# Optimization experiments

Measured on AMD Instinct MI355X. Metric: run time of the kernel, lower is better.

## Reference

```python
import jax, jax.numpy as jnp
import numpy as np

B, N, D, H, K = 32, 256, 256, 8, 16
EPS = 1e-8
SINK_EPS = 1e-6
SINK_ITERS = 10
TAU_SLOT = 0.5
G_TEMP = 1.0
FROB_LAMBDA = 0.02
ORTH_LAMBDA = 0.1
USAGE_LAMBDA = 0.1


def _xavier(key, shape, fan_in, fan_out):
    bound = np.sqrt(6.0 / (fan_in + fan_out))
    return jax.random.uniform(key, shape, jnp.float32, -bound, bound)


def setup_inputs() -> dict:
    key = jax.random.key(0)
    k0, k1, k2, k3, k4 = jax.random.split(key, 5)
    return {
        "desc_embeddings": jax.random.normal(k0, (B, N, D), jnp.float32),
        "name_value_embeddings": jax.random.normal(k1, (B, N, D), jnp.float32),
        "W_fusion": _xavier(k2, (D, 2 * D), 2 * D, D),   # torch Linear weight [out,in]
        "b_fusion": jnp.zeros((D,), jnp.float32),
        "W_slot": _xavier(k3, (K, D), D, K),
        "b_slot": jnp.zeros((K,), jnp.float32),
        "G_param": _xavier(k4, (H, K, K), K * K, H * K),
    }


def _sinkhorn(M, iters=SINK_ITERS, eps=SINK_EPS):
    M = jnp.maximum(M, eps)
    for _ in range(iters):  # fixed small iter count
        M = M / (M.sum(axis=-1, keepdims=True) + eps)
        M = M / (M.sum(axis=-2, keepdims=True) + eps)
    return M


def _forward(desc, nv, W_fusion, b_fusion, W_slot, b_slot, G_param):
    # fusion + slot assignment  S: [B,N,K]
    z = jnp.concatenate([desc, nv], axis=-1) @ W_fusion.T + b_fusion
    S = jax.nn.softmax(z @ W_slot.T + b_slot, axis=-1)

    # global slot-transition matrices  G: [H,K,K]
    G = jax.nn.softmax(G_param / G_TEMP, axis=-1)
    G = _sinkhorn(G)
    G = G * (1.0 - jnp.eye(K, dtype=G.dtype))  # zero diagonal

    # Frobenius diversity regularizer across heads
    V = G.reshape(H, -1)
    V = V / jnp.maximum(jnp.linalg.norm(V, axis=1, keepdims=True), 1e-8)
    Gram = V @ V.T
    g_reg = FROB_LAMBDA * (Gram.sum() - jnp.trace(Gram)) / (H * (H - 1))

    # slot-bilinear affinity  A: [B,H,N,N]
    SG = jnp.einsum('bnk,hkl->bhnl', S, G)
    A_slot = jnp.einsum('bhnl,bml->bhnm', SG, S)
    Q = jax.nn.softmax(A_slot / max(TAU_SLOT, 1e-6), axis=-1)

    # slot orthogonality regularizer
    StS = jnp.einsum('bnk,bnl->bkl', S, S) / float(N)
    offdiag = StS * (1.0 - jnp.eye(K, dtype=S.dtype))
    reg_orth = ORTH_LAMBDA * jnp.mean(offdiag ** 2)

    # slot usage KL(u || uniform)
    u = S.mean(axis=1)
    u = u / (u.sum(axis=-1, keepdims=True) + EPS)
    uc = jnp.maximum(u, EPS)
    usage_kl = jnp.mean(jnp.sum(uc * (jnp.log(uc) - jnp.log(jnp.float32(1.0 / K))), axis=-1))
    reg_usage = USAGE_LAMBDA * usage_kl

    total_reg = reg_orth + reg_usage + g_reg
    bias_log = jax.lax.stop_gradient(jnp.log(jnp.maximum(Q, EPS)))
    return bias_log, Q, total_reg


def reference(desc_embeddings, name_value_embeddings, W_fusion, b_fusion, W_slot, b_slot, G_param):
    return _forward(desc_embeddings, name_value_embeddings, W_fusion, b_fusion, W_slot, b_slot, G_param)
```

## Files before the change

kernel.cpp:

```cpp
#include <hip/hip_runtime.h>
#include <math.h>

#define LOG_EPS   (-18.420680743952367f)
#define LOG_INV_K (-2.772588722239781f)

__global__ void kA(const float* __restrict__ W_fusion, const float* __restrict__ b_fusion,
                   const float* __restrict__ W_slot,   const float* __restrict__ b_slot,
                   const float* __restrict__ G_param,
                   float* __restrict__ W_eff, float* __restrict__ b_eff,
                   float* __restrict__ G_out, float* __restrict__ out_reg) {
    int t = threadIdx.x;
    if (blockIdx.x < 32) {
        int idx = blockIdx.x * 256 + t;
        int k = idx >> 9, j = idx & 511;
        const float* ws = W_slot + k * 256;
        float s = 0.f;
        #pragma unroll 4
        for (int d = 0; d < 256; ++d) s += ws[d] * W_fusion[d * 512 + j];
        W_eff[idx] = s;
        if (idx < 16) {
            float bb = b_slot[idx];
            for (int d = 0; d < 256; ++d) bb += W_slot[idx * 256 + d] * b_fusion[d];
            b_eff[idx] = bb;
        }
        return;
    }
    __shared__ float M[2048];
    __shared__ float red[256];
    __shared__ float inv_nrm[8];
    __shared__ float hsq[8];
    __shared__ float trace_s;

    if (t < 128) {
        int base = t * 16;
        float v[16]; float mx = -1e30f;
        #pragma unroll
        for (int l = 0; l < 16; ++l) { v[l] = G_param[base + l]; mx = fmaxf(mx, v[l]); }
        float s = 0.f;
        #pragma unroll
        for (int l = 0; l < 16; ++l) { v[l] = expf(v[l] - mx); s += v[l]; }
        float r = 1.f / s;
        #pragma unroll
        for (int l = 0; l < 16; ++l) M[base + l] = fmaxf(v[l] * r, 1e-6f);
    }
    __syncthreads();
    for (int it = 0; it < 10; ++it) {
        if (t < 128) {
            float s = 0.f;
            #pragma unroll
            for (int l = 0; l < 16; ++l) s += M[t * 16 + l];
            float r = 1.f / (s + 1e-6f);
            #pragma unroll
            for (int l = 0; l < 16; ++l) M[t * 16 + l] *= r;
        }
        __syncthreads();
        if (t < 128) {
            int h = t >> 4, l = t & 15, base = h * 256 + l;
            float s = 0.f;
            #pragma unroll
            for (int k = 0; k < 16; ++k) s += M[base + k * 16];
            float r = 1.f / (s + 1e-6f);
            #pragma unroll
            for (int k = 0; k < 16; ++k) M[base + k * 16] *= r;
        }
        __syncthreads();
    }
    if (t < 128) { int h = t >> 4, k = t & 15; M[h * 256 + k * 16 + k] = 0.f; }
    __syncthreads();
    for (int i = t; i < 2048; i += 256) G_out[i] = M[i];

    if (t < 128) {
        float s = 0.f;
        #pragma unroll
        for (int l = 0; l < 16; ++l) { float x = M[t * 16 + l]; s += x * x; }
        red[t] = s;
    }
    __syncthreads();
    if (t < 8) {
        float s = 0.f;
        for (int k = 0; k < 16; ++k) s += red[t * 16 + k];
        float inv = 1.f / fmaxf(sqrtf(s), 1e-8f);
        inv_nrm[t] = inv;
        hsq[t] = s * inv * inv;
    }
    __syncthreads();
    if (t == 0) {
        float tr = 0.f;
        for (int h = 0; h < 8; ++h) tr += hsq[h];
        trace_s = tr;
    }
    __syncthreads();
    float w = 0.f;
    #pragma unroll
    for (int h = 0; h < 8; ++h) w += M[h * 256 + t] * inv_nrm[h];
    red[t] = w * w;
    __syncthreads();
    for (int off = 128; off; off >>= 1) {
        if (t < off) red[t] += red[t + off];
        __syncthreads();
    }
    if (t == 0) out_reg[0] = 0.02f * (red[0] - trace_s) / 56.f;
}

__global__ void kB(const float* __restrict__ desc, const float* __restrict__ nv,
                   const float* __restrict__ W_eff, const float* __restrict__ b_eff,
                   float* __restrict__ S) {
    int row  = blockIdx.x * 4 + (threadIdx.x >> 6);
    int lane = threadIdx.x & 63;
    int k = lane & 15, q = lane >> 4;
    const float* x = (q < 2) ? (desc + (size_t)row * 256 + q * 128)
                             : (nv   + (size_t)row * 256 + (q - 2) * 128);
    const float4* x4 = (const float4*)x;
    const float4* w4 = (const float4*)(W_eff + k * 512 + q * 128);
    float acc = 0.f;
    #pragma unroll
    for (int i = 0; i < 32; ++i) {
        float4 a = x4[i], b = w4[i];
        acc += a.x * b.x + a.y * b.y + a.z * b.z + a.w * b.w;
    }
    acc += __shfl_xor(acc, 16);
    acc += __shfl_xor(acc, 32);
    float logit = acc + b_eff[k];
    float mx = logit;
    #pragma unroll
    for (int off = 8; off; off >>= 1) mx = fmaxf(mx, __shfl_xor(mx, off));
    float e = __expf(logit - mx);
    float s = e;
    #pragma unroll
    for (int off = 8; off; off >>= 1) s += __shfl_xor(s, off);
    if (q == 0) S[(size_t)row * 16 + k] = e / s;
}

__global__ __launch_bounds__(256) void kC(const float* __restrict__ S,
                                          const float* __restrict__ G,
                                          float* __restrict__ bias,
                                          float* __restrict__ Q,
                                          float* __restrict__ out_reg) {
    __shared__ float Sl[4096];
    __shared__ float Gl[256];
    __shared__ float Rp[64 * 17];
    __shared__ float Ru[64 * 16];
    __shared__ float pmax[256], psum[256];
    __shared__ float rmx[64], rln[64], rrc[64];
    int t = threadIdx.x;
    int blk = blockIdx.x;

    if (blk >= 1024) {
        int b = blk - 1024;
        for (int i = t; i < 4096; i += 256) Sl[i] = S[(size_t)b * 4096 + i];
        __syncthreads();
        int k = t >> 4, l = t & 15;
        float s = 0.f;
        for (int n = 0; n < 256; ++n) s += Sl[n * 16 + k] * Sl[n * 16 + l];
        s *= (1.f / 256.f);
        pmax[t] = (k == l) ? 0.f : s * s;
        __syncthreads();
        for (int off = 128; off; off >>= 1) {
            if (t < off) pmax[t] += pmax[t + off];
            __syncthreads();
        }
        if (t < 16) {
            float u = 0.f;
            for (int n = 0; n < 256; ++n) u += Sl[n * 16 + t];
            psum[t] = u * (1.f / 256.f);
        }
        __syncthreads();
        if (t == 0) {
            float su = 0.f;
            for (int kk = 0; kk < 16; ++kk) su += psum[kk];
            float kl = 0.f;
            for (int kk = 0; kk < 16; ++kk) {
                float uc = fmaxf(psum[kk] / (su + 1e-8f), 1e-8f);
                kl += uc * (logf(uc) - LOG_INV_K);
            }
            float val = 0.1f * pmax[0] / 8192.f + 0.1f * kl / 32.f;
            atomicAdd(out_reg, val);
        }
        return;
    }

    int bh = blk >> 2, qq = blk & 3;
    int b = bh >> 3, h = bh & 7;
    int n0 = qq * 64;

    const float4* Sg = (const float4*)(S + (size_t)b * 4096);
    float4* Sl4 = (float4*)Sl;
    for (int i = t; i < 1024; i += 256) Sl4[i] = Sg[i];
    Gl[t] = G[h * 256 + t];
    __syncthreads();

    for (int i = t; i < 1024; i += 256) {
        int r = i >> 4, l = i & 15;
        float s = 0.f;
        #pragma unroll
        for (int k = 0; k < 16; ++k) s += Sl[(n0 + r) * 16 + k] * Gl[k * 16 + l];
        Rp[r * 17 + l] = s;
        Ru[r * 16 + l] = s;
    }
    __syncthreads();

    {
        int r = t & 63, seg = t >> 6;
        float rreg[16];
        #pragma unroll
        for (int l = 0; l < 16; ++l) rreg[l] = Rp[r * 17 + l];
        float mx = -1e30f, ls = 0.f;
        const float4* Srow = (const float4*)(Sl + seg * 64 * 16);
        for (int m = 0; m < 64; ++m) {
            float4 s0 = Srow[m * 4 + 0], s1 = Srow[m * 4 + 1];
            float4 s2 = Srow[m * 4 + 2], s3 = Srow[m * 4 + 3];
            float a = rreg[0] * s0.x + rreg[1] * s0.y + rreg[2] * s0.z + rreg[3] * s0.w
                    + rreg[4] * s1.x + rreg[5] * s1.y + rreg[6] * s1.z + rreg[7] * s1.w
                    + rreg[8] * s2.x + rreg[9] * s2.y + rreg[10] * s2.z + rreg[11] * s2.w
                    + rreg[12] * s3.x + rreg[13] * s3.y + rreg[14] * s3.z + rreg[15] * s3.w;
            float x = 2.f * a;
            float nm = fmaxf(mx, x);
            ls = ls * __expf(mx - nm) + __expf(x - nm);
            mx = nm;
        }
        pmax[t] = mx;
        psum[t] = ls;
    }
    __syncthreads();
    if (t < 64) {
        float m0 = pmax[t], m1 = pmax[64 + t], m2 = pmax[128 + t], m3 = pmax[192 + t];
        float M = fmaxf(fmaxf(m0, m1), fmaxf(m2, m3));
        float L = psum[t] * __expf(m0 - M) + psum[64 + t] * __expf(m1 - M)
                + psum[128 + t] * __expf(m2 - M) + psum[192 + t] * __expf(m3 - M);
        rmx[t] = M;
        rln[t] = __logf(L);
        rrc[t] = 1.f / L;
    }
    __syncthreads();

    {
        int cg = t & 63, rs = t >> 6;
        float sr[4][16];
        #pragma unroll
        for (int j = 0; j < 4; ++j) {
            const float4* p = (const float4*)(Sl + (4 * cg + j) * 16);
            float4 a = p[0], c = p[1], d = p[2], e = p[3];
            sr[j][0]=a.x; sr[j][1]=a.y; sr[j][2]=a.z; sr[j][3]=a.w;
            sr[j][4]=c.x; sr[j][5]=c.y; sr[j][6]=c.z; sr[j][7]=c.w;
            sr[j][8]=d.x; sr[j][9]=d.y; sr[j][10]=d.z; sr[j][11]=d.w;
            sr[j][12]=e.x; sr[j][13]=e.y; sr[j][14]=e.z; sr[j][15]=e.w;
        }
        size_t base = (size_t)bh * 65536;
        for (int rr = rs; rr < 64; rr += 4) {
            int n = n0 + rr;
            const float4* rp = (const float4*)(Ru + rr * 16);
            float4 r0 = rp[0], r1 = rp[1], r2 = rp[2], r3 = rp[3];
            float rv[16] = { r0.x,r0.y,r0.z,r0.w, r1.x,r1.y,r1.z,r1.w,
                             r2.x,r2.y,r2.z,r2.w, r3.x,r3.y,r3.z,r3.w };
            float m_ = rmx[rr], lnl = rln[rr], rc = rrc[rr];
            float4 qv, bv;
            float* qp = (float*)&qv;
            float* bp = (float*)&bv;
            #pragma unroll
            for (int j = 0; j < 4; ++j) {
                float a = 0.f;
                #pragma unroll
                for (int l = 0; l < 16; ++l) a += rv[l] * sr[j][l];
                float xm = 2.f * a - m_;
                qp[j] = __expf(xm) * rc;
                bp[j] = fmaxf(xm - lnl, LOG_EPS);
            }
            *(float4*)(Q    + base + (size_t)n * 256 + 4 * cg) = qv;
            *(float4*)(bias + base + (size_t)n * 256 + 4 * cg) = bv;
        }
    }
}

extern "C" void kernel_launch(void* const* d_in, const int* in_sizes, int n_in,
                              void* d_out, int out_size, void* d_ws, size_t ws_size,
                              hipStream_t stream) {
    const float* desc     = (const float*)d_in[0];
    const float* nv       = (const float*)d_in[1];
    const float* W_fusion = (const float*)d_in[2];
    const float* b_fusion = (const float*)d_in[3];
    const float* W_slot   = (const float*)d_in[4];
    const float* b_slot   = (const float*)d_in[5];
    const float* G_param  = (const float*)d_in[6];

    float* out = (float*)d_out;
    float* out_bias = out;
    float* out_Q    = out + 16777216;
    float* out_reg  = out + 33554432;

    float* ws    = (float*)d_ws;
    float* W_eff = ws;
    float* b_eff = ws + 8192;
    float* G_out = ws + 8208;
    float* S     = ws + 10256;

    kA<<<33, 256, 0, stream>>>(W_fusion, b_fusion, W_slot, b_slot, G_param,
                               W_eff, b_eff, G_out, out_reg);
    kB<<<2048, 256, 0, stream>>>(desc, nv, W_eff, b_eff, S);
    kC<<<1056, 256, 0, stream>>>(S, G_out, out_bias, out_Q, out_reg);
}
```

Before: 250.8 us.

## Compute slot affinity logits once in registers and skip softmax max subtraction

The Q/bias kernel now computes each thread's 64 logits once and keeps them in registers. It sums their exponentials directly, with no running max, and reuses the stored logits to write Q and bias. Before, it computed the bilinear dot products twice: once for an online max/sum pass and once for the output pass. Dropping the max relies on the logits being bounded (S and G entries are at most 1), and the factor 2 is folded into the precomputed S·G rows, removing half the FMAs and several reduction and sync steps. In exchange, each thread now writes a contiguous 256-byte stretch of one row instead of coalesced float4 columns across a row, which may hurt store coalescing. Register pressure also rises, capped by launch bounds of 4 blocks.

```diff
diff --git a/kernel.cpp b/kernel.cpp
--- a/kernel.cpp
+++ b/kernel.cpp
@@ -131,37 +131,36 @@
     if (q == 0) S[(size_t)row * 16 + k] = e / s;
 }
 
-__global__ __launch_bounds__(256) void kC(const float* __restrict__ S,
-                                          const float* __restrict__ G,
-                                          float* __restrict__ bias,
-                                          float* __restrict__ Q,
-                                          float* __restrict__ out_reg) {
-    __shared__ float Sl[4096];
+__global__ __launch_bounds__(256, 4) void kC(const float* __restrict__ S,
+                                             const float* __restrict__ G,
+                                             float* __restrict__ bias,
+                                             float* __restrict__ Q,
+                                             float* __restrict__ out_reg) {
+    __shared__ float Su[4096];
     __shared__ float Gl[256];
-    __shared__ float Rp[64 * 17];
-    __shared__ float Ru[64 * 16];
-    __shared__ float pmax[256], psum[256];
-    __shared__ float rmx[64], rln[64], rrc[64];
+    __shared__ float Rl[64 * 20];
+    __shared__ float psum[256];
+    __shared__ float red[256];
     int t = threadIdx.x;
     int blk = blockIdx.x;
 
     if (blk >= 1024) {
         int b = blk - 1024;
-        for (int i = t; i < 4096; i += 256) Sl[i] = S[(size_t)b * 4096 + i];
+        for (int i = t; i < 4096; i += 256) Su[i] = S[(size_t)b * 4096 + i];
         __syncthreads();
         int k = t >> 4, l = t & 15;
         float s = 0.f;
-        for (int n = 0; n < 256; ++n) s += Sl[n * 16 + k] * Sl[n * 16 + l];
+        for (int n = 0; n < 256; ++n) s += Su[n * 16 + k] * Su[n * 16 + l];
         s *= (1.f / 256.f);
-        pmax[t] = (k == l) ? 0.f : s * s;
+        red[t] = (k == l) ? 0.f : s * s;
         __syncthreads();
         for (int off = 128; off; off >>= 1) {
-            if (t < off) pmax[t] += pmax[t + off];
+            if (t < off) red[t] += red[t + off];
             __syncthreads();
         }
         if (t < 16) {
             float u = 0.f;
-            for (int n = 0; n < 256; ++n) u += Sl[n * 16 + t];
+            for (int n = 0; n < 256; ++n) u += Su[n * 16 + t];
             psum[t] = u * (1.f / 256.f);
         }
         __syncthreads();
@@ -173,7 +172,7 @@
                 float uc = fmaxf(psum[kk] / (su + 1e-8f), 1e-8f);
                 kl += uc * (logf(uc) - LOG_INV_K);
             }
-            float val = 0.1f * pmax[0] / 8192.f + 0.1f * kl / 32.f;
+            float val = 0.1f * red[0] / 8192.f + 0.1f * kl / 32.f;
             atomicAdd(out_reg, val);
         }
         return;
@@ -183,91 +182,76 @@
     int b = bh >> 3, h = bh & 7;
     int n0 = qq * 64;
 
-    const float4* Sg = (const float4*)(S + (size_t)b * 4096);
-    float4* Sl4 = (float4*)Sl;
-    for (int i = t; i < 1024; i += 256) Sl4[i] = Sg[i];
-    Gl[t] = G[h * 256 + t];
-    __syncthreads();
-
-    for (int i = t; i < 1024; i += 256) {
-        int r = i >> 4, l = i & 15;
-        float s = 0.f;
-        #pragma unroll
-        for (int k = 0; k < 16; ++k) s += Sl[(n0 + r) * 16 + k] * Gl[k * 16 + l];
-        Rp[r * 17 + l] = s;
-        Ru[r * 16 + l] = s;
-    }
-    __syncthreads();
-
     {
-        int r = t & 63, seg = t >> 6;
-        float rreg[16];
-        #pragma unroll
-        for (int l = 0; l < 16; ++l) rreg[l] = Rp[r * 17 + l];
-        float mx = -1e30f, ls = 0.f;
-        const float4* Srow = (const float4*)(Sl + seg * 64 * 16);
-        for (int m = 0; m < 64; ++m) {
-            float4 s0 = Srow[m * 4 + 0], s1 = Srow[m * 4 + 1];
-            float4 s2 = Srow[m * 4 + 2], s3 = Srow[m * 4 + 3];
-            float a = rreg[0] * s0.x + rreg[1] * s0.y + rreg[2] * s0.z + rreg[3] * s0.w
-                    + rreg[4] * s1.x + rreg[5] * s1.y + rreg[6] * s1.z + rreg[7] * s1.w
-                    + rreg[8] * s2.x + rreg[9] * s2.y + rreg[10] * s2.z + rreg[11] * s2.w
-                    + rreg[12] * s3.x + rreg[13] * s3.y + rreg[14] * s3.z + rreg[15] * s3.w;
-            float x = 2.f * a;
-            float nm = fmaxf(mx, x);
-            ls = ls * __expf(mx - nm) + __expf(x - nm);
-            mx = nm;
-        }
-        pmax[t] = mx;
-        psum[t] = ls;
-    }
-    __syncthreads();
-    if (t < 64) {
-        float m0 = pmax[t], m1 = pmax[64 + t], m2 = pmax[128 + t], m3 = pmax[192 + t];
-        float M = fmaxf(fmaxf(m0, m1), fmaxf(m2, m3));
-        float L = psum[t] * __expf(m0 - M) + psum[64 + t] * __expf(m1 - M)
-                + psum[128 + t] * __expf(m2 - M) + psum[192 + t] * __expf(m3 - M);
-        rmx[t] = M;
-        rln[t] = __logf(L);
-        rrc[t] = 1.f / L;
+        const float4* Sg = (const float4*)(S + (size_t)b * 4096);
+        float4* Su4 = (float4*)Su;
+        for (int i = t; i < 1024; i += 256) Su4[i] = Sg[i];
+        Gl[t] = G[h * 256 + t];
     }
     __syncthreads();
 
     {
-        int cg = t & 63, rs = t >> 6;
-        float sr[4][16];
-        #pragma unroll
-        for (int j = 0; j < 4; ++j) {
-            const float4* p = (const float4*)(Sl + (4 * cg + j) * 16);
-            float4 a = p[0], c = p[1], d = p[2], e = p[3];
-            sr[j][0]=a.x; sr[j][1]=a.y; sr[j][2]=a.z; sr[j][3]=a.w;
-            sr[j][4]=c.x; sr[j][5]=c.y; sr[j][6]=c.z; sr[j][7]=c.w;
-            sr[j][8]=d.x; sr[j][9]=d.y; sr[j][10]=d.z; sr[j][11]=d.w;
-            sr[j][12]=e.x; sr[j][13]=e.y; sr[j][14]=e.z; sr[j][15]=e.w;
-        }
-        size_t base = (size_t)bh * 65536;
-        for (int rr = rs; rr < 64; rr += 4) {
-            int n = n0 + rr;
-            const float4* rp = (const float4*)(Ru + rr * 16);
-            float4 r0 = rp[0], r1 = rp[1], r2 = rp[2], r3 = rp[3];
-            float rv[16] = { r0.x,r0.y,r0.z,r0.w, r1.x,r1.y,r1.z,r1.w,
-                             r2.x,r2.y,r2.z,r2.w, r3.x,r3.y,r3.z,r3.w };
-            float m_ = rmx[rr], lnl = rln[rr], rc = rrc[rr];
-            float4 qv, bv;
-            float* qp = (float*)&qv;
-            float* bp = (float*)&bv;
-            #pragma unroll
-            for (int j = 0; j < 4; ++j) {
-                float a = 0.f;
-                #pragma unroll
-                for (int l = 0; l < 16; ++l) a += rv[l] * sr[j][l];
-                float xm = 2.f * a - m_;
-                qp[j] = __expf(xm) * rc;
-                bp[j] = fmaxf(xm - lnl, LOG_EPS);
-            }
-            *(float4*)(Q    + base + (size_t)n * 256 + 4 * cg) = qv;
-            *(float4*)(bias + base + (size_t)n * 256 + 4 * cg) = bv;
-        }
+        int r = t >> 2, l4 = (t & 3) * 4;
+        const float4* mp = (const float4*)(S + (size_t)b * 4096 + (size_t)(n0 + r) * 16);
+        float4 s0 = mp[0], s1 = mp[1], s2 = mp[2], s3 = mp[3];
+        float sr[16] = { s0.x,s0.y,s0.z,s0.w, s1.x,s1.y,s1.z,s1.w,
+                         s2.x,s2.y,s2.z,s2.w, s3.x,s3.y,s3.z,s3.w };
+        float a0 = 0.f, a1 = 0.f, a2 = 0.f, a3 = 0.f;
+        #pragma unroll
+        for (int k = 0; k < 16; ++k) {
+            float4 g = *(const float4*)(Gl + k * 16 + l4);
+            a0 += sr[k] * g.x; a1 += sr[k] * g.y;
+            a2 += sr[k] * g.z; a3 += sr[k] * g.w;
+        }
+        float4 rv = make_float4(2.f * a0, 2.f * a1, 2.f * a2, 2.f * a3);
+        *(float4*)(Rl + r * 20 + l4) = rv;
+    }
+    __syncthreads();
+
+    int r = t & 63, w = t >> 6;
+    float rv[16];
+    {
+        const float4* rp = (const float4*)(Rl + r * 20);
+        float4 r0 = rp[0], r1 = rp[1], r2 = rp[2], r3 = rp[3];
+        rv[0]=r0.x; rv[1]=r0.y; rv[2]=r0.z; rv[3]=r0.w;
+        rv[4]=r1.x; rv[5]=r1.y; rv[6]=r1.z; rv[7]=r1.w;
+        rv[8]=r2.x; rv[9]=r2.y; rv[10]=r2.z; rv[11]=r2.w;
+        rv[12]=r3.x; rv[13]=r3.y; rv[14]=r3.z; rv[15]=r3.w;
+    }
+
+    int mbase = w * 64;
+    float a[64];
+    float ls = 0.f;
+    #pragma unroll
+    for (int j = 0; j < 64; ++j) {
+        const float4* p = (const float4*)(Su + (mbase + j) * 16);
+        float4 q0 = p[0], q1 = p[1], q2 = p[2], q3 = p[3];
+        float x = rv[0]*q0.x + rv[1]*q0.y + rv[2]*q0.z + rv[3]*q0.w
+                + rv[4]*q1.x + rv[5]*q1.y + rv[6]*q1.z + rv[7]*q1.w
+                + rv[8]*q2.x + rv[9]*q2.y + rv[10]*q2.z + rv[11]*q2.w
+                + rv[12]*q3.x + rv[13]*q3.y + rv[14]*q3.z + rv[15]*q3.w;
+        a[j] = x;
+        ls += __expf(x);
+    }
+    psum[t] = ls;
+    __syncthreads();
+
+    float L = psum[r] + psum[64 + r] + psum[128 + r] + psum[192 + r];
+    float lnL = __logf(L);
+    float rc = 1.f / L;
+
+    size_t base = (size_t)bh * 65536 + (size_t)(n0 + r) * 256 + mbase;
+    float4* Qp = (float4*)(Q + base);
+    float4* Bp = (float4*)(bias + base);
+    #pragma unroll
+    for (int j4 = 0; j4 < 16; ++j4) {
+        float4 qv, bv;
+        qv.x = __expf(a[4*j4+0]) * rc;  bv.x = fmaxf(a[4*j4+0] - lnL, LOG_EPS);
+        qv.y = __expf(a[4*j4+1]) * rc;  bv.y = fmaxf(a[4*j4+1] - lnL, LOG_EPS);
+        qv.z = __expf(a[4*j4+2]) * rc;  bv.z = fmaxf(a[4*j4+2] - lnL, LOG_EPS);
+        qv.w = __expf(a[4*j4+3]) * rc;  bv.w = fmaxf(a[4*j4+3] - lnL, LOG_EPS);
+        Qp[j4] = qv;
+        Bp[j4] = bv;
     }
 }
 
```

Measured after the change: 355.3 us. +41.7%, slower.
